# Kernel optimization log

Measured on AMD Instinct MI355X. Metric: run time of the kernel, lower is better.

The kernel has to match this reference:

```python
import jax, jax.numpy as jnp
import numpy as np

BS, L, D, CACHE = 8, 2048, 2048, 64   # sequences, tokens/seq, embed_dim, cache rows
T = BS * L
EPS = 1e-6


def setup_inputs() -> dict:
    key = jax.random.key(0)
    ks = jax.random.split(key, 7)
    inputs = jax.random.normal(ks[0], (T, D), jnp.float32)
    lf1_caches = jax.random.normal(ks[1], (CACHE, D), jnp.float32)
    lf2_caches = jax.random.normal(ks[2], (CACHE, D // 2), jnp.float32)
    conv1_weight = jax.random.normal(ks[3], (D, D), jnp.float32) * 0.02
    conv2_weight = jax.random.normal(ks[4], (D // 2, 2 * D), jnp.float32) * 0.02
    conv1_bias = jax.random.normal(ks[5], (D // 2,), jnp.float32) * 0.02
    conv2_bias = jax.random.normal(ks[6], (D,), jnp.float32) * 0.02
    ln_weight = jnp.ones((D,), jnp.float32)
    # consistent continuous-batching layout: each sequence s occupies rows
    # [s*(L+1) .. s*(L+1)+L] of the padded buffer: [cache_tok, tok0..tok_{L-1}]
    s = np.arange(BS, dtype=np.int64)
    j = np.arange(L, dtype=np.int64)
    pre_lf_indexs = jnp.asarray(s)                                  # cache slot per seq
    out_lf_indexs = jnp.asarray(s)
    input_lf_loc = jnp.asarray(s * (L + 1))                         # where cache row goes
    out_lf_loc = jnp.asarray(s * (L + 1) + L)                       # last token -> cache
    inputs_loc = jnp.asarray((s[:, None] * (L + 1) + 1 + j[None, :]).reshape(-1))
    outputs_loc = jnp.asarray((s[:, None] * (L + 1) + j[None, :]).reshape(-1))
    return {
        "inputs": inputs, "pre_lf_indexs": pre_lf_indexs, "out_lf_indexs": out_lf_indexs,
        "input_lf_loc": input_lf_loc, "out_lf_loc": out_lf_loc,
        "inputs_loc": inputs_loc, "outputs_loc": outputs_loc,
        "lf1_caches": lf1_caches, "lf2_caches": lf2_caches,
        "conv1_weight": conv1_weight, "conv2_weight": conv2_weight,
        "conv1_bias": conv1_bias, "conv2_bias": conv2_bias, "ln_weight": ln_weight,
    }


def _fused_cat_conv2d(x, cache, pre_idx, in_lf_loc, in_loc, out_loc, W):
    # scatter tokens + gathered cache rows into padded buffer [T+bs, d]
    bs = pre_idx.shape[0]
    xt = jnp.zeros((x.shape[0] + bs, x.shape[1]), x.dtype)
    xt = xt.at[in_loc].set(x).at[in_lf_loc].set(cache[pre_idx])
    c = xt @ W                                  # [T+bs, 2h]
    h = c.shape[1] // 2
    y = c[:-1, :h] + c[1:, h:]                  # kernel-2 causal conv via shift-add
    return y[out_loc]                           # [T, h]


def reference(inputs, pre_lf_indexs, out_lf_indexs, input_lf_loc, out_lf_loc,
              inputs_loc, outputs_loc, lf1_caches, lf2_caches,
              conv1_weight, conv2_weight, conv1_bias, conv2_bias, ln_weight):
    o1 = _fused_cat_conv2d(inputs, lf1_caches, pre_lf_indexs, input_lf_loc,
                           inputs_loc, outputs_loc, conv1_weight) + conv1_bias
    o2 = _fused_cat_conv2d(o1, lf2_caches, pre_lf_indexs, input_lf_loc,
                           inputs_loc, outputs_loc, conv2_weight) + conv2_bias
    o3 = o2 + inputs
    var = jnp.mean(o3 * o3, axis=-1, keepdims=True)          # RMSNorm
    return o3 * jax.lax.rsqrt(var + EPS) * ln_weight
```

## Files before the change

### kernel.cpp

```cpp
#include <hip/hip_runtime.h>
#include <hip/hip_bf16.h>
#include <stdint.h>

#define T_TOK   16384
#define BSQ     8
#define MROWS   16392
#define D1      2048
#define D2      1024

typedef __attribute__((ext_vector_type(8))) short bf16x8;
typedef __attribute__((ext_vector_type(4))) float f32x4;

__device__ __forceinline__ void gll16(const void* g, void* l) {
  __builtin_amdgcn_global_load_lds(
      (const __attribute__((address_space(1))) void*)g,
      (__attribute__((address_space(3))) void*)l, 16, 0, 0);
}

__global__ __launch_bounds__(256) void transpose_cvt2(
    const float* __restrict__ in, __hip_bfloat16* __restrict__ out,
    int Cin, int ldout, int c0, int kout0) {
  __shared__ float tile[32][33];
  int bx = blockIdx.x * 32;
  int by = blockIdx.y * 32;
  int tx = threadIdx.x, ty = threadIdx.y;
  #pragma unroll
  for (int i = 0; i < 32; i += 8)
    tile[ty + i][tx] = in[(size_t)(by + ty + i) * Cin + c0 + bx + tx];
  __syncthreads();
  #pragma unroll
  for (int i = 0; i < 32; i += 8)
    out[(size_t)(bx + ty + i) * ldout + kout0 + by + tx] =
        __float2bfloat16(tile[tx][ty + i]);
}

__global__ __launch_bounds__(256) void scatter_tokens(
    const float* __restrict__ x, const int* __restrict__ loc,
    __hip_bfloat16* __restrict__ xt) {
  int t = blockIdx.x;
  int c = threadIdx.x * 8;
  int r = loc[t];
  const float* src = x + (size_t)t * 2048 + c;
  float4 v0 = *(const float4*)src;
  float4 v1 = *(const float4*)(src + 4);
  union { __hip_bfloat16 h[8]; uint4 u; } o;
  o.h[0] = __float2bfloat16(v0.x); o.h[1] = __float2bfloat16(v0.y);
  o.h[2] = __float2bfloat16(v0.z); o.h[3] = __float2bfloat16(v0.w);
  o.h[4] = __float2bfloat16(v1.x); o.h[5] = __float2bfloat16(v1.y);
  o.h[6] = __float2bfloat16(v1.z); o.h[7] = __float2bfloat16(v1.w);
  *(uint4*)(xt + (size_t)r * 2048 + c) = o.u;
}

__global__ __launch_bounds__(256) void cachepad(
    const float* __restrict__ cache, const int* __restrict__ pre,
    const int* __restrict__ lfloc, __hip_bfloat16* __restrict__ xt, int cols) {
  int r = blockIdx.x;
  int dst = lfloc[r];
  const float* src = cache + (size_t)pre[r] * cols;
  for (int c = threadIdx.x; c < cols; c += 256)
    xt[(size_t)dst * cols + c] = __float2bfloat16(src[c]);
}

template <int EPI>
__global__ __launch_bounds__(256, 2) void gemm_conv(
    const __hip_bfloat16* __restrict__ A0,
    const __hip_bfloat16* __restrict__ Bt,
    const float* __restrict__ bias,
    const float* __restrict__ resid,
    __hip_bfloat16* __restrict__ outb,
    float* __restrict__ outf,
    int N, int K, int KH, int ldA) {
  __shared__ __align__(16) __hip_bfloat16 sA[128 * 32];
  __shared__ __align__(16) __hip_bfloat16 sB[128 * 32];
  const int tid = threadIdx.x;
  const int wave = tid >> 6, lane = tid & 63;
  const int wm = wave & 1, wn = wave >> 1;
  const int tn = blockIdx.x, tm = blockIdx.y;
  const int s = tm >> 4;
  const size_t r0 = (size_t)tm * 128 + s;

  const __hip_bfloat16* A0r = A0 + r0 * ldA;
  const __hip_bfloat16* A1r = A0 + (r0 + 1) * ldA;
  const __hip_bfloat16* Bb = Bt + (size_t)tn * 128 * K;

  const int srow = wave * 16 + (lane >> 2);
  const int scol = (lane & 3) * 8;

  f32x4 acc[4][4];
  #pragma unroll
  for (int i = 0; i < 4; ++i)
    #pragma unroll
    for (int j = 0; j < 4; ++j)
      #pragma unroll
      for (int e = 0; e < 4; ++e) acc[i][j][e] = 0.0f;

  const int frow = lane & 15;
  const int fk = (lane >> 4) * 8;

  for (int k0 = 0; k0 < K; k0 += 32) {
    const __hip_bfloat16* Abase =
        (k0 < KH) ? (A0r + k0) : (A1r + (k0 - KH));
    gll16(Abase + (size_t)srow * ldA + scol,        sA + (wave * 16) * 32);
    gll16(Abase + (size_t)(64 + srow) * ldA + scol, sA + (64 + wave * 16) * 32);
    gll16(Bb + (size_t)srow * K + k0 + scol,        sB + (wave * 16) * 32);
    gll16(Bb + (size_t)(64 + srow) * K + k0 + scol, sB + (64 + wave * 16) * 32);
    __builtin_amdgcn_s_waitcnt(0);
    __syncthreads();

    bf16x8 af[4], bfr[4];
    #pragma unroll
    for (int i = 0; i < 4; ++i)
      af[i] = *(const bf16x8*)(sA + (wm * 64 + i * 16 + frow) * 32 + fk);
    #pragma unroll
    for (int j = 0; j < 4; ++j)
      bfr[j] = *(const bf16x8*)(sB + (wn * 64 + j * 16 + frow) * 32 + fk);
    #pragma unroll
    for (int i = 0; i < 4; ++i)
      #pragma unroll
      for (int j = 0; j < 4; ++j)
        acc[i][j] = __builtin_amdgcn_mfma_f32_16x16x32_bf16(af[i], bfr[j], acc[i][j], 0, 0, 0);
    __syncthreads();
  }

  const int t0 = tm * 128 + wm * 64 + (lane >> 4) * 4;
  const int ccol = tn * 128 + wn * 64 + (lane & 15);
  float bj[4];
  #pragma unroll
  for (int j = 0; j < 4; ++j) bj[j] = bias[ccol + j * 16];

  #pragma unroll
  for (int i = 0; i < 4; ++i)
    #pragma unroll
    for (int p = 0; p < 4; ++p) {
      int t = t0 + i * 16 + p;
      if (EPI == 1) {
        __hip_bfloat16* dst = outb + ((size_t)t + s + 1) * N + ccol;
        #pragma unroll
        for (int j = 0; j < 4; ++j)
          dst[j * 16] = __float2bfloat16(acc[i][j][p] + bj[j]);
      } else {
        const float* rsrc = resid + (size_t)t * N + ccol;
        float* dst = outf + (size_t)t * N + ccol;
        #pragma unroll
        for (int j = 0; j < 4; ++j)
          dst[j * 16] = acc[i][j][p] + bj[j] + rsrc[j * 16];
      }
    }
}

__global__ __launch_bounds__(256) void rmsnorm(
    const float* __restrict__ o3, const float* __restrict__ lnw,
    float* __restrict__ out) {
  __shared__ float red[4];
  int t = blockIdx.x;
  int d = threadIdx.x * 8;
  const float* p = o3 + (size_t)t * 2048 + d;
  float o[8];
  *(float4*)&o[0] = *(const float4*)p;
  *(float4*)&o[4] = *(const float4*)(p + 4);
  float ss = 0.0f;
  #pragma unroll
  for (int k = 0; k < 8; ++k) ss += o[k] * o[k];
  #pragma unroll
  for (int off = 32; off > 0; off >>= 1) ss += __shfl_down(ss, off, 64);
  if ((threadIdx.x & 63) == 0) red[threadIdx.x >> 6] = ss;
  __syncthreads();
  float tot = red[0] + red[1] + red[2] + red[3];
  float sc = rsqrtf(tot * (1.0f / 2048.0f) + 1e-6f);
  float lw[8], res[8];
  *(float4*)&lw[0] = *(const float4*)(lnw + d);
  *(float4*)&lw[4] = *(const float4*)(lnw + d + 4);
  #pragma unroll
  for (int k = 0; k < 8; ++k) res[k] = o[k] * sc * lw[k];
  float* dst = out + (size_t)t * 2048 + d;
  *(float4*)dst = *(float4*)&res[0];
  *(float4*)(dst + 4) = *(float4*)&res[4];
}

extern "C" void kernel_launch(void* const* d_in, const int* in_sizes, int n_in,
                              void* d_out, int out_size, void* d_ws, size_t ws_size,
                              hipStream_t stream) {
  const float* inputs = (const float*)d_in[0];
  const int* pre_idx  = (const int*)d_in[1];
  const int* in_lf_loc = (const int*)d_in[3];
  const int* in_loc  = (const int*)d_in[5];
  const float* lf1 = (const float*)d_in[7];
  const float* lf2 = (const float*)d_in[8];
  const float* W1 = (const float*)d_in[9];
  const float* W2 = (const float*)d_in[10];
  const float* b1 = (const float*)d_in[11];
  const float* b2 = (const float*)d_in[12];
  const float* lnw = (const float*)d_in[13];
  float* out = (float*)d_out;

  char* ws = (char*)d_ws;
  float* o3 = (float*)ws;
  __hip_bfloat16* xt1 = (__hip_bfloat16*)(ws + 134217728ull);
  __hip_bfloat16* xt2 = (__hip_bfloat16*)(ws + 201359360ull);
  __hip_bfloat16* bt1 = (__hip_bfloat16*)(ws + 234930176ull);
  __hip_bfloat16* bt2 = (__hip_bfloat16*)(ws + 243318784ull);

  transpose_cvt2<<<dim3(32, 64), dim3(32, 8), 0, stream>>>(W1, bt1, 2048, 4096, 0, 0);
  transpose_cvt2<<<dim3(32, 64), dim3(32, 8), 0, stream>>>(W1, bt1, 2048, 4096, 1024, 2048);
  transpose_cvt2<<<dim3(64, 32), dim3(32, 8), 0, stream>>>(W2, bt2, 4096, 2048, 0, 0);
  transpose_cvt2<<<dim3(64, 32), dim3(32, 8), 0, stream>>>(W2, bt2, 4096, 2048, 2048, 1024);

  scatter_tokens<<<T_TOK, 256, 0, stream>>>(inputs, in_loc, xt1);
  cachepad<<<BSQ, 256, 0, stream>>>(lf1, pre_idx, in_lf_loc, xt1, 2048);
  cachepad<<<BSQ, 256, 0, stream>>>(lf2, pre_idx, in_lf_loc, xt2, 1024);

  gemm_conv<1><<<dim3(8, 128), 256, 0, stream>>>(
      xt1, bt1, b1, nullptr, xt2, nullptr, 1024, 4096, 2048, 2048);

  gemm_conv<2><<<dim3(16, 128), 256, 0, stream>>>(
      xt2, bt2, b2, inputs, nullptr, o3, 2048, 2048, 1024, 1024);

  rmsnorm<<<T_TOK, 256, 0, stream>>>(o3, lnw, out);
}
```

Before: 691.1 us.

## Merge prologue launches, split GEMM K-loop by segment, raise occupancy bound

```diff
diff --git a/kernel.cpp b/kernel.cpp
--- a/kernel.cpp
+++ b/kernel.cpp
@@ -4,7 +4,6 @@
 
 #define T_TOK   16384
 #define BSQ     8
-#define MROWS   16392
 #define D1      2048
 #define D2      1024
 
@@ -17,52 +16,69 @@
       (__attribute__((address_space(3))) void*)l, 16, 0, 0);
 }
 
-__global__ __launch_bounds__(256) void transpose_cvt2(
-    const float* __restrict__ in, __hip_bfloat16* __restrict__ out,
-    int Cin, int ldout, int c0, int kout0) {
+__global__ __launch_bounds__(256) void transpose_all(
+    const float* __restrict__ W1, const float* __restrict__ W2,
+    __hip_bfloat16* __restrict__ bt1, __hip_bfloat16* __restrict__ bt2) {
   __shared__ float tile[32][33];
-  int bx = blockIdx.x * 32;
-  int by = blockIdx.y * 32;
+  int job = blockIdx.x >> 11;
+  int i = blockIdx.x & 2047;
+  const float* in; __hip_bfloat16* out;
+  int Cin, ldout, c0, kout0, bx, by;
+  if (job < 2) {
+    in = W1; out = bt1; Cin = 2048; ldout = 4096;
+    c0 = job ? 1024 : 0; kout0 = job ? 2048 : 0;
+    bx = (i & 31) * 32; by = (i >> 5) * 32;
+  } else {
+    in = W2; out = bt2; Cin = 4096; ldout = 2048;
+    c0 = (job == 3) ? 2048 : 0; kout0 = (job == 3) ? 1024 : 0;
+    bx = (i & 63) * 32; by = (i >> 6) * 32;
+  }
   int tx = threadIdx.x, ty = threadIdx.y;
   #pragma unroll
-  for (int i = 0; i < 32; i += 8)
-    tile[ty + i][tx] = in[(size_t)(by + ty + i) * Cin + c0 + bx + tx];
+  for (int q = 0; q < 32; q += 8)
+    tile[ty + q][tx] = in[(size_t)(by + ty + q) * Cin + c0 + bx + tx];
   __syncthreads();
   #pragma unroll
-  for (int i = 0; i < 32; i += 8)
-    out[(size_t)(bx + ty + i) * ldout + kout0 + by + tx] =
-        __float2bfloat16(tile[tx][ty + i]);
-}
-
-__global__ __launch_bounds__(256) void scatter_tokens(
+  for (int q = 0; q < 32; q += 8)
+    out[(size_t)(bx + ty + q) * ldout + kout0 + by + tx] =
+        __float2bfloat16(tile[tx][ty + q]);
+}
+
+__global__ __launch_bounds__(256) void prologue(
     const float* __restrict__ x, const int* __restrict__ loc,
-    __hip_bfloat16* __restrict__ xt) {
-  int t = blockIdx.x;
-  int c = threadIdx.x * 8;
-  int r = loc[t];
-  const float* src = x + (size_t)t * 2048 + c;
-  float4 v0 = *(const float4*)src;
-  float4 v1 = *(const float4*)(src + 4);
-  union { __hip_bfloat16 h[8]; uint4 u; } o;
-  o.h[0] = __float2bfloat16(v0.x); o.h[1] = __float2bfloat16(v0.y);
-  o.h[2] = __float2bfloat16(v0.z); o.h[3] = __float2bfloat16(v0.w);
-  o.h[4] = __float2bfloat16(v1.x); o.h[5] = __float2bfloat16(v1.y);
-  o.h[6] = __float2bfloat16(v1.z); o.h[7] = __float2bfloat16(v1.w);
-  *(uint4*)(xt + (size_t)r * 2048 + c) = o.u;
-}
-
-__global__ __launch_bounds__(256) void cachepad(
-    const float* __restrict__ cache, const int* __restrict__ pre,
-    const int* __restrict__ lfloc, __hip_bfloat16* __restrict__ xt, int cols) {
-  int r = blockIdx.x;
-  int dst = lfloc[r];
-  const float* src = cache + (size_t)pre[r] * cols;
-  for (int c = threadIdx.x; c < cols; c += 256)
-    xt[(size_t)dst * cols + c] = __float2bfloat16(src[c]);
+    const float* __restrict__ lf1, const float* __restrict__ lf2,
+    const int* __restrict__ pre, const int* __restrict__ lfloc,
+    __hip_bfloat16* __restrict__ xt1, __hip_bfloat16* __restrict__ xt2) {
+  int b = blockIdx.x;
+  if (b < T_TOK) {
+    int c = threadIdx.x * 8;
+    int r = loc[b];
+    const float* src = x + (size_t)b * 2048 + c;
+    float4 v0 = *(const float4*)src;
+    float4 v1 = *(const float4*)(src + 4);
+    union { __hip_bfloat16 h[8]; uint4 u; } o;
+    o.h[0] = __float2bfloat16(v0.x); o.h[1] = __float2bfloat16(v0.y);
+    o.h[2] = __float2bfloat16(v0.z); o.h[3] = __float2bfloat16(v0.w);
+    o.h[4] = __float2bfloat16(v1.x); o.h[5] = __float2bfloat16(v1.y);
+    o.h[6] = __float2bfloat16(v1.z); o.h[7] = __float2bfloat16(v1.w);
+    *(uint4*)(xt1 + (size_t)r * 2048 + c) = o.u;
+  } else if (b < T_TOK + BSQ) {
+    int s = b - T_TOK;
+    int dst = lfloc[s];
+    const float* src = lf1 + (size_t)pre[s] * 2048;
+    for (int c = threadIdx.x; c < 2048; c += 256)
+      xt1[(size_t)dst * 2048 + c] = __float2bfloat16(src[c]);
+  } else {
+    int s = b - T_TOK - BSQ;
+    int dst = lfloc[s];
+    const float* src = lf2 + (size_t)pre[s] * 1024;
+    for (int c = threadIdx.x; c < 1024; c += 256)
+      xt2[(size_t)dst * 1024 + c] = __float2bfloat16(src[c]);
+  }
 }
 
 template <int EPI>
-__global__ __launch_bounds__(256, 2) void gemm_conv(
+__global__ __launch_bounds__(256, 4) void gemm_conv(
     const __hip_bfloat16* __restrict__ A0,
     const __hip_bfloat16* __restrict__ Bt,
     const float* __restrict__ bias,
@@ -79,8 +95,6 @@
   const int s = tm >> 4;
   const size_t r0 = (size_t)tm * 128 + s;
 
-  const __hip_bfloat16* A0r = A0 + r0 * ldA;
-  const __hip_bfloat16* A1r = A0 + (r0 + 1) * ldA;
   const __hip_bfloat16* Bb = Bt + (size_t)tn * 128 * K;
 
   const int srow = wave * 16 + (lane >> 2);
@@ -97,29 +111,33 @@
   const int frow = lane & 15;
   const int fk = (lane >> 4) * 8;
 
-  for (int k0 = 0; k0 < K; k0 += 32) {
-    const __hip_bfloat16* Abase =
-        (k0 < KH) ? (A0r + k0) : (A1r + (k0 - KH));
-    gll16(Abase + (size_t)srow * ldA + scol,        sA + (wave * 16) * 32);
-    gll16(Abase + (size_t)(64 + srow) * ldA + scol, sA + (64 + wave * 16) * 32);
-    gll16(Bb + (size_t)srow * K + k0 + scol,        sB + (wave * 16) * 32);
-    gll16(Bb + (size_t)(64 + srow) * K + k0 + scol, sB + (64 + wave * 16) * 32);
-    __builtin_amdgcn_s_waitcnt(0);
-    __syncthreads();
-
-    bf16x8 af[4], bfr[4];
-    #pragma unroll
-    for (int i = 0; i < 4; ++i)
-      af[i] = *(const bf16x8*)(sA + (wm * 64 + i * 16 + frow) * 32 + fk);
-    #pragma unroll
-    for (int j = 0; j < 4; ++j)
-      bfr[j] = *(const bf16x8*)(sB + (wn * 64 + j * 16 + frow) * 32 + fk);
-    #pragma unroll
-    for (int i = 0; i < 4; ++i)
+  #pragma unroll 1
+  for (int seg = 0; seg < 2; ++seg) {
+    const __hip_bfloat16* Ar = A0 + (r0 + seg) * ldA;
+    const __hip_bfloat16* Bs = Bb + seg * KH;
+    #pragma unroll 1
+    for (int k0 = 0; k0 < KH; k0 += 32) {
+      gll16(Ar + (size_t)srow * ldA + k0 + scol,        sA + (wave * 16) * 32);
+      gll16(Ar + (size_t)(64 + srow) * ldA + k0 + scol, sA + (64 + wave * 16) * 32);
+      gll16(Bs + (size_t)srow * K + k0 + scol,          sB + (wave * 16) * 32);
+      gll16(Bs + (size_t)(64 + srow) * K + k0 + scol,   sB + (64 + wave * 16) * 32);
+      __builtin_amdgcn_s_waitcnt(0);
+      __syncthreads();
+
+      bf16x8 af[4], bfr[4];
+      #pragma unroll
+      for (int i = 0; i < 4; ++i)
+        af[i] = *(const bf16x8*)(sA + (wm * 64 + i * 16 + frow) * 32 + fk);
       #pragma unroll
       for (int j = 0; j < 4; ++j)
-        acc[i][j] = __builtin_amdgcn_mfma_f32_16x16x32_bf16(af[i], bfr[j], acc[i][j], 0, 0, 0);
-    __syncthreads();
+        bfr[j] = *(const bf16x8*)(sB + (wn * 64 + j * 16 + frow) * 32 + fk);
+      #pragma unroll
+      for (int i = 0; i < 4; ++i)
+        #pragma unroll
+        for (int j = 0; j < 4; ++j)
+          acc[i][j] = __builtin_amdgcn_mfma_f32_16x16x32_bf16(af[i], bfr[j], acc[i][j], 0, 0, 0);
+      __syncthreads();
+    }
   }
 
   const int t0 = tm * 128 + wm * 64 + (lane >> 4) * 4;
@@ -200,14 +218,9 @@
   __hip_bfloat16* bt1 = (__hip_bfloat16*)(ws + 234930176ull);
   __hip_bfloat16* bt2 = (__hip_bfloat16*)(ws + 243318784ull);
 
-  transpose_cvt2<<<dim3(32, 64), dim3(32, 8), 0, stream>>>(W1, bt1, 2048, 4096, 0, 0);
-  transpose_cvt2<<<dim3(32, 64), dim3(32, 8), 0, stream>>>(W1, bt1, 2048, 4096, 1024, 2048);
-  transpose_cvt2<<<dim3(64, 32), dim3(32, 8), 0, stream>>>(W2, bt2, 4096, 2048, 0, 0);
-  transpose_cvt2<<<dim3(64, 32), dim3(32, 8), 0, stream>>>(W2, bt2, 4096, 2048, 2048, 1024);
-
-  scatter_tokens<<<T_TOK, 256, 0, stream>>>(inputs, in_loc, xt1);
-  cachepad<<<BSQ, 256, 0, stream>>>(lf1, pre_idx, in_lf_loc, xt1, 2048);
-  cachepad<<<BSQ, 256, 0, stream>>>(lf2, pre_idx, in_lf_loc, xt2, 1024);
+  transpose_all<<<8192, dim3(32, 8), 0, stream>>>(W1, W2, bt1, bt2);
+  prologue<<<T_TOK + 2 * BSQ, 256, 0, stream>>>(
+      inputs, in_loc, lf1, lf2, pre_idx, in_lf_loc, xt1, xt2);
 
   gemm_conv<1><<<dim3(8, 128), 256, 0, stream>>>(
       xt1, bt1, b1, nullptr, xt2, nullptr, 1024, 4096, 2048, 2048);
```

New measurement: 682.6 us. No clear change (-1.2%).
